# Optimization experiments

Hardware: AMD Instinct MI355X
Metric: run time of the kernel (lower is better)

The kernel has to match this reference:

```python
import jax, jax.numpy as jnp
import numpy as np

D_MODEL = 2048
BOTTLENECK = 64
EPS = 1e-5  # torch LayerNorm default


def setup_inputs() -> dict:
    key = jax.random.key(0)
    k = jax.random.split(key, 7)
    x = jax.random.normal(k[0], (4, 4096, D_MODEL), dtype=jnp.float32)
    # LayerNorm params
    ln_gamma = jnp.ones((D_MODEL,), dtype=jnp.float32)
    ln_beta = jnp.zeros((D_MODEL,), dtype=jnp.float32)
    # down_proj: Linear(d_model -> bottleneck); torch weight shape [out, in]
    w_down = jax.random.normal(k[1], (BOTTLENECK, D_MODEL), dtype=jnp.float32) * (1.0 / np.sqrt(D_MODEL))
    b_down = jax.random.normal(k[2], (BOTTLENECK,), dtype=jnp.float32) * 0.01
    # up_proj: Linear(bottleneck -> d_model)
    w_up = jax.random.normal(k[3], (D_MODEL, BOTTLENECK), dtype=jnp.float32) * (1.0 / np.sqrt(BOTTLENECK))
    b_up = jax.random.normal(k[4], (D_MODEL,), dtype=jnp.float32) * 0.01
    return {"x": x, "ln_gamma": ln_gamma, "ln_beta": ln_beta,
            "w_down": w_down, "b_down": b_down, "w_up": w_up, "b_up": b_up}


def reference(x, ln_gamma, ln_beta, w_down, b_down, w_up, b_up):
    # adapter_layernorm_option == 'in': LayerNorm first
    mu = jnp.mean(x, axis=-1, keepdims=True)
    var = jnp.mean(jnp.square(x - mu), axis=-1, keepdims=True)
    xn = (x - mu) * jax.lax.rsqrt(var + EPS) * ln_gamma + ln_beta
    # down-proj -> ReLU -> up-proj (scale/dropout are never applied in forward)
    down = jnp.maximum(jnp.einsum('bsd,kd->bsk', xn, w_down) + b_down, 0.0)
    out = jnp.einsum('bsk,dk->bsd', down, w_up) + b_up
    return out
```

## Files before the change

kernel.cpp:

```cpp
#include <hip/hip_runtime.h>


typedef __attribute__((ext_vector_type(8))) short short8;
typedef __attribute__((ext_vector_type(4))) float f32x4;

#define D_MODEL 2048
#define BNECK   64
#define EPS     1e-5f
#define NCHUNK  32

__device__ inline short f2bf(float f) {
    unsigned int u = __builtin_bit_cast(unsigned int, f);
    unsigned int r = (u + 0x7fffu + ((u >> 16) & 1u)) >> 16;
    return (short)r;
}
__device__ inline float bf2f(short s) {
    unsigned int u = ((unsigned int)(unsigned short)s) << 16;
    return __builtin_bit_cast(float, u);
}

__global__ __launch_bounds__(256) void prep_kernel(
    const float* __restrict__ w_down, const float* __restrict__ gamma,
    const float* __restrict__ beta,   const float* __restrict__ b_down,
    const float* __restrict__ w_up,
    short* __restrict__ wg_perm, short* __restrict__ wup_perm,
    float* __restrict__ s_out, float* __restrict__ c_out)
{
    __shared__ float rs[4], rc[4];
    int b = blockIdx.x;
    if (b < BNECK) {
        int n = b, nf = n >> 4;
        float ps = 0.f, pc = 0.f;
        for (int d = threadIdx.x; d < D_MODEL; d += 256) {
            float wv = w_down[n * D_MODEL + d];
            short h  = f2bf(wv * gamma[d]);
            int t = d >> 5, kg = (d >> 3) & 3, e = d & 7;
            int l = kg * 16 + (n & 15);
            wg_perm[(size_t)((nf * 64 + t) * 64 + l) * 8 + e] = h;
            ps += bf2f(h);
            pc  = fmaf(wv, beta[d], pc);
        }
        for (int o = 32; o > 0; o >>= 1) {
            ps += __shfl_down(ps, o, 64);
            pc += __shfl_down(pc, o, 64);
        }
        int wid = threadIdx.x >> 6, lane = threadIdx.x & 63;
        if (lane == 0) { rs[wid] = ps; rc[wid] = pc; }
        __syncthreads();
        if (threadIdx.x == 0) {
            s_out[n] = rs[0] + rs[1] + rs[2] + rs[3];
            c_out[n] = rc[0] + rc[1] + rc[2] + rc[3] + b_down[n];
        }
    } else {
        for (int j = (b - BNECK) * 256 + threadIdx.x; j < D_MODEL * BNECK;
             j += 64 * 256) {
            int d = j >> 6, kn = j & 63;
            int b16 = d >> 4, h2 = kn >> 5, e = kn & 7;
            int l = ((kn >> 3) & 3) * 16 + (d & 15);
            wup_perm[(size_t)((b16 * 2 + h2) * 64 + l) * 8 + e] = f2bf(w_up[j]);
        }
    }
}

__global__ __launch_bounds__(256, 4) void adapter_kernel(
    const float* __restrict__ x,    const float* __restrict__ b_up,
    const short* __restrict__ wg_perm, const short* __restrict__ wup_perm,
    const float* __restrict__ s_v,  const float* __restrict__ c_v,
    float* __restrict__ out)
{
    __shared__ __align__(16) char xbuf[2][4096];
    __shared__ __align__(16) char tilebuf[2048];
    __shared__ float stats2[16][2];

    const int wid  = threadIdx.x >> 6;
    const int lane = threadIdx.x & 63;
    const int r    = lane & 15;
    const int g    = lane >> 4;
    const int row0 = blockIdx.x * 16;
    const int swz  = (r & 7) << 4;

    const int srow = wid * 4 + g;
    const int scol = r * 16;
    const char* xsrc = (const char*)x
        + ((size_t)(row0 + srow) * D_MODEL) * 4 + scol;
    char* const swdst = &xbuf[0][0] + srow * 256 + (scol ^ ((srow & 7) << 4));

    const short* wbase = wg_perm + (size_t)(wid * 64) * 512 + lane * 8;

    f32x4  xr[4];
    short8 wb[2][2];
    f32x4  acc = (f32x4){0.f, 0.f, 0.f, 0.f};
    float  ssum = 0.f, ssq = 0.f;

    auto LDX = [&](int c) { return *(const f32x4*)(xsrc + c * 256); };
    auto LDW = [&](int c, short8* w) {
        w[0] = *(const short8*)(wbase + (size_t)(c * 2 + 0) * 512);
        w[1] = *(const short8*)(wbase + (size_t)(c * 2 + 1) * 512);
    };
    auto STATS_WRITE = [&](int c, const f32x4& v) {
        ssum += (v.x + v.y) + (v.z + v.w);
        ssq = fmaf(v.x, v.x, ssq); ssq = fmaf(v.y, v.y, ssq);
        ssq = fmaf(v.z, v.z, ssq); ssq = fmaf(v.w, v.w, ssq);
        *(f32x4*)(swdst + (size_t)(c & 1) * 4096) = v;
    };

    xr[0] = LDX(0); xr[1] = LDX(1); xr[2] = LDX(2);
    LDW(0, wb[0]);
    STATS_WRITE(0, xr[0]);

#pragma unroll
    for (int c = 0; c < NCHUNK; ++c) {
        if (c + 3 < NCHUNK) xr[(c + 3) & 3] = LDX(c + 3);
        if (c + 1 < NCHUNK) LDW(c + 1, wb[(c + 1) & 1]);
        asm volatile("s_waitcnt lgkmcnt(0)\n\ts_barrier" ::: "memory");
        if (c + 1 < NCHUNK) STATS_WRITE(c + 1, xr[(c + 1) & 3]);

        const char* bp = &xbuf[c & 1][0];
        const short8* w = wb[c & 1];
#pragma unroll
        for (int kb = 0; kb < 2; ++kb) {
            int cb = kb * 128 + g * 32;
            f32x4 xa = *(const f32x4*)(bp + r * 256 + ( cb        ^ swz));
            f32x4 xb = *(const f32x4*)(bp + r * 256 + ((cb + 16)  ^ swz));
            short8 af;
            af[0] = f2bf(xa.x); af[1] = f2bf(xa.y);
            af[2] = f2bf(xa.z); af[3] = f2bf(xa.w);
            af[4] = f2bf(xb.x); af[5] = f2bf(xb.y);
            af[6] = f2bf(xb.z); af[7] = f2bf(xb.w);
            acc = __builtin_amdgcn_mfma_f32_16x16x32_bf16(af, w[kb], acc, 0, 0, 0);
        }
    }

#pragma unroll
    for (int m = 1; m < 16; m <<= 1) {
        ssum += __shfl_xor(ssum, m, 64);
        ssq  += __shfl_xor(ssq , m, 64);
    }
    float mu   = ssum * (1.f / D_MODEL);
    float rstd = rsqrtf(ssq * (1.f / D_MODEL) - mu * mu + EPS);
    if (r == 0) { stats2[srow][0] = mu; stats2[srow][1] = rstd; }
    __syncthreads();

    {
        int   n  = wid * 16 + r;
        float sn = s_v[n], cn = c_v[n];
#pragma unroll
        for (int reg = 0; reg < 4; ++reg) {
            int   m = g * 4 + reg;
            float v = fmaf(stats2[m][1], acc[reg] - stats2[m][0] * sn, cn);
            v = fmaxf(v, 0.f);
            *(short*)(tilebuf + ((m * 128 + n * 2) ^ ((m & 7) << 4))) = f2bf(v);
        }
    }
    __syncthreads();

    short8 bd0 = *(const short8*)(tilebuf + ((r * 128 +  0 + g * 16) ^ swz));
    short8 bd1 = *(const short8*)(tilebuf + ((r * 128 + 64 + g * 16) ^ swz));

    const short* wupl = wup_perm + lane * 8;
    float* outr = out + (size_t)(row0 + r) * D_MODEL;

    short8 ua[2], ub[2];
    {
        int b16 = wid * 32;
        ua[0] = *(const short8*)(wupl + (size_t)(b16 * 2 + 0) * 512);
        ub[0] = *(const short8*)(wupl + (size_t)(b16 * 2 + 1) * 512);
    }
#pragma unroll
    for (int i = 0; i < 32; ++i) {
        int cur = i & 1;
        if (i < 31) {
            int b16 = wid * 32 + i + 1;
            ua[cur ^ 1] = *(const short8*)(wupl + (size_t)(b16 * 2 + 0) * 512);
            ub[cur ^ 1] = *(const short8*)(wupl + (size_t)(b16 * 2 + 1) * 512);
        }
        f32x4 o = (f32x4){0.f, 0.f, 0.f, 0.f};
        o = __builtin_amdgcn_mfma_f32_16x16x32_bf16(ua[cur], bd0, o, 0, 0, 0);
        o = __builtin_amdgcn_mfma_f32_16x16x32_bf16(ub[cur], bd1, o, 0, 0, 0);
        int dbase = (wid * 32 + i) * 16;
        f32x4 bu = *(const f32x4*)(b_up + dbase + g * 4);
        o += bu;
        *(f32x4*)(outr + dbase + g * 4) = o;
    }
}

extern "C" void kernel_launch(void* const* d_in, const int* in_sizes, int n_in,
                              void* d_out, int out_size, void* d_ws, size_t ws_size,
                              hipStream_t stream) {
    const float* x      = (const float*)d_in[0];
    const float* gamma  = (const float*)d_in[1];
    const float* beta   = (const float*)d_in[2];
    const float* w_down = (const float*)d_in[3];
    const float* b_down = (const float*)d_in[4];
    const float* w_up   = (const float*)d_in[5];
    const float* b_up   = (const float*)d_in[6];
    float* out = (float*)d_out;

    char* ws = (char*)d_ws;
    short* wg_perm  = (short*)ws;
    short* wup_perm = (short*)(ws + 262144);
    float* s_v  = (float*)(ws + 524288);
    float* c_v  = (float*)(ws + 524544);

    prep_kernel<<<128, 256, 0, stream>>>(w_down, gamma, beta, b_down, w_up,
                                         wg_perm, wup_perm, s_v, c_v);
    adapter_kernel<<<1024, 256, 0, stream>>>(x, b_up, wg_perm, wup_perm,
                                             s_v, c_v, out);
}
```

Baseline: 67.99 us.

## Process 32 rows per block to reuse weight fragments across two M tiles

Each block now handles 32 rows instead of 16, with two MFMA accumulators that share each loaded down-projection and up-projection weight fragment. This halves weight traffic per row and halves the grid to 512 blocks. The bf16 conversion also switches to the HIP library intrinsic, which may map to a hardware convert instruction. In exchange, each block uses twice the LDS and more registers, which could lower occupancy, and 512 blocks gives fewer waves to hide latency on a 256-CU device.

Result: slower. 71.21 us (+4.7%).

```diff
diff --git a/kernel.cpp b/kernel.cpp
--- a/kernel.cpp
+++ b/kernel.cpp
@@ -1,4 +1,5 @@
 #include <hip/hip_runtime.h>
+#include <hip/hip_bf16.h>
 
 
 typedef __attribute__((ext_vector_type(8))) short short8;
@@ -17,6 +18,16 @@
 __device__ inline float bf2f(short s) {
     unsigned int u = ((unsigned int)(unsigned short)s) << 16;
     return __builtin_bit_cast(float, u);
+}
+__device__ inline short hbf(float f) {
+    __hip_bfloat16 h = __float2bfloat16(f);
+    return __builtin_bit_cast(short, h);
+}
+__device__ inline short8 cvt8(const f32x4& a, const f32x4& b) {
+    short8 o;
+    o[0] = hbf(a.x); o[1] = hbf(a.y); o[2] = hbf(a.z); o[3] = hbf(a.w);
+    o[4] = hbf(b.x); o[5] = hbf(b.y); o[6] = hbf(b.z); o[7] = hbf(b.w);
+    return o;
 }
 
 __global__ __launch_bounds__(256) void prep_kernel(
@@ -68,49 +79,59 @@
     const float* __restrict__ s_v,  const float* __restrict__ c_v,
     float* __restrict__ out)
 {
-    __shared__ __align__(16) char xbuf[2][4096];
-    __shared__ __align__(16) char tilebuf[2048];
-    __shared__ float stats2[16][2];
+    __shared__ __align__(16) char xbuf[2][8192];
+    __shared__ __align__(16) char tilebuf[4096];
+    __shared__ float stats2[32][2];
 
     const int wid  = threadIdx.x >> 6;
     const int lane = threadIdx.x & 63;
     const int r    = lane & 15;
     const int g    = lane >> 4;
-    const int row0 = blockIdx.x * 16;
+    const int row0 = blockIdx.x * 32;
     const int swz  = (r & 7) << 4;
 
-    const int srow = wid * 4 + g;
-    const int scol = r * 16;
+    const int sr  = wid * 8 + g * 2 + (r >> 3);
+    const int scb = (r & 7) * 32;
     const char* xsrc = (const char*)x
-        + ((size_t)(row0 + srow) * D_MODEL) * 4 + scol;
-    char* const swdst = &xbuf[0][0] + srow * 256 + (scol ^ ((srow & 7) << 4));
+        + ((size_t)(row0 + sr) * D_MODEL) * 4 + scb;
+    const int swr = (sr & 7) << 4;
+    char* const swdst0 = &xbuf[0][0] + sr * 256 + ( scb       ^ swr);
+    char* const swdst1 = &xbuf[0][0] + sr * 256 + ((scb + 16) ^ swr);
 
     const short* wbase = wg_perm + (size_t)(wid * 64) * 512 + lane * 8;
 
-    f32x4  xr[4];
+    f32x4  xr[4][2];
     short8 wb[2][2];
-    f32x4  acc = (f32x4){0.f, 0.f, 0.f, 0.f};
+    f32x4  acc0 = (f32x4){0.f, 0.f, 0.f, 0.f};
+    f32x4  acc1 = (f32x4){0.f, 0.f, 0.f, 0.f};
     float  ssum = 0.f, ssq = 0.f;
 
-    auto LDX = [&](int c) { return *(const f32x4*)(xsrc + c * 256); };
+    auto LDX = [&](int c, f32x4* o) {
+        o[0] = *(const f32x4*)(xsrc + c * 256);
+        o[1] = *(const f32x4*)(xsrc + c * 256 + 16);
+    };
     auto LDW = [&](int c, short8* w) {
         w[0] = *(const short8*)(wbase + (size_t)(c * 2 + 0) * 512);
         w[1] = *(const short8*)(wbase + (size_t)(c * 2 + 1) * 512);
     };
-    auto STATS_WRITE = [&](int c, const f32x4& v) {
-        ssum += (v.x + v.y) + (v.z + v.w);
-        ssq = fmaf(v.x, v.x, ssq); ssq = fmaf(v.y, v.y, ssq);
-        ssq = fmaf(v.z, v.z, ssq); ssq = fmaf(v.w, v.w, ssq);
-        *(f32x4*)(swdst + (size_t)(c & 1) * 4096) = v;
+    auto STATS_WRITE = [&](int c, const f32x4* v) {
+#pragma unroll
+        for (int h = 0; h < 2; ++h) {
+            ssum += (v[h].x + v[h].y) + (v[h].z + v[h].w);
+            ssq = fmaf(v[h].x, v[h].x, ssq); ssq = fmaf(v[h].y, v[h].y, ssq);
+            ssq = fmaf(v[h].z, v[h].z, ssq); ssq = fmaf(v[h].w, v[h].w, ssq);
+        }
+        *(f32x4*)(swdst0 + (size_t)(c & 1) * 8192) = v[0];
+        *(f32x4*)(swdst1 + (size_t)(c & 1) * 8192) = v[1];
     };
 
-    xr[0] = LDX(0); xr[1] = LDX(1); xr[2] = LDX(2);
+    LDX(0, xr[0]); LDX(1, xr[1]); LDX(2, xr[2]);
     LDW(0, wb[0]);
     STATS_WRITE(0, xr[0]);
 
 #pragma unroll
     for (int c = 0; c < NCHUNK; ++c) {
-        if (c + 3 < NCHUNK) xr[(c + 3) & 3] = LDX(c + 3);
+        if (c + 3 < NCHUNK) LDX(c + 3, xr[(c + 3) & 3]);
         if (c + 1 < NCHUNK) LDW(c + 1, wb[(c + 1) & 1]);
         asm volatile("s_waitcnt lgkmcnt(0)\n\ts_barrier" ::: "memory");
         if (c + 1 < NCHUNK) STATS_WRITE(c + 1, xr[(c + 1) & 3]);
@@ -120,45 +141,53 @@
 #pragma unroll
         for (int kb = 0; kb < 2; ++kb) {
             int cb = kb * 128 + g * 32;
-            f32x4 xa = *(const f32x4*)(bp + r * 256 + ( cb        ^ swz));
-            f32x4 xb = *(const f32x4*)(bp + r * 256 + ((cb + 16)  ^ swz));
-            short8 af;
-            af[0] = f2bf(xa.x); af[1] = f2bf(xa.y);
-            af[2] = f2bf(xa.z); af[3] = f2bf(xa.w);
-            af[4] = f2bf(xb.x); af[5] = f2bf(xb.y);
-            af[6] = f2bf(xb.z); af[7] = f2bf(xb.w);
-            acc = __builtin_amdgcn_mfma_f32_16x16x32_bf16(af, w[kb], acc, 0, 0, 0);
-        }
-    }
-
-#pragma unroll
-    for (int m = 1; m < 16; m <<= 1) {
+            f32x4 xa0 = *(const f32x4*)(bp + r * 256        + ( cb       ^ swz));
+            f32x4 xb0 = *(const f32x4*)(bp + r * 256        + ((cb + 16) ^ swz));
+            f32x4 xa1 = *(const f32x4*)(bp + (16 + r) * 256 + ( cb       ^ swz));
+            f32x4 xb1 = *(const f32x4*)(bp + (16 + r) * 256 + ((cb + 16) ^ swz));
+            acc0 = __builtin_amdgcn_mfma_f32_16x16x32_bf16(cvt8(xa0, xb0), w[kb], acc0, 0, 0, 0);
+            acc1 = __builtin_amdgcn_mfma_f32_16x16x32_bf16(cvt8(xa1, xb1), w[kb], acc1, 0, 0, 0);
+        }
+    }
+
+#pragma unroll
+    for (int m = 1; m < 8; m <<= 1) {
         ssum += __shfl_xor(ssum, m, 64);
         ssq  += __shfl_xor(ssq , m, 64);
     }
     float mu   = ssum * (1.f / D_MODEL);
     float rstd = rsqrtf(ssq * (1.f / D_MODEL) - mu * mu + EPS);
-    if (r == 0) { stats2[srow][0] = mu; stats2[srow][1] = rstd; }
+    if ((r & 7) == 0) { stats2[sr][0] = mu; stats2[sr][1] = rstd; }
     __syncthreads();
 
     {
         int   n  = wid * 16 + r;
         float sn = s_v[n], cn = c_v[n];
 #pragma unroll
-        for (int reg = 0; reg < 4; ++reg) {
-            int   m = g * 4 + reg;
-            float v = fmaf(stats2[m][1], acc[reg] - stats2[m][0] * sn, cn);
-            v = fmaxf(v, 0.f);
-            *(short*)(tilebuf + ((m * 128 + n * 2) ^ ((m & 7) << 4))) = f2bf(v);
+        for (int mb = 0; mb < 2; ++mb) {
+            const f32x4& a = mb ? acc1 : acc0;
+#pragma unroll
+            for (int reg = 0; reg < 4; ++reg) {
+                int   m = mb * 16 + g * 4 + reg;
+                float v = fmaf(stats2[m][1], a[reg] - stats2[m][0] * sn, cn);
+                v = fmaxf(v, 0.f);
+                *(short*)(tilebuf + ((m * 128 + n * 2) ^ ((m & 7) << 4))) = hbf(v);
+            }
         }
     }
     __syncthreads();
 
-    short8 bd0 = *(const short8*)(tilebuf + ((r * 128 +  0 + g * 16) ^ swz));
-    short8 bd1 = *(const short8*)(tilebuf + ((r * 128 + 64 + g * 16) ^ swz));
+    short8 bd[2][2];
+#pragma unroll
+    for (int tb = 0; tb < 2; ++tb) {
+        int t = tb * 16 + r;
+        bd[tb][0] = *(const short8*)(tilebuf + ((t * 128 +  0 + g * 16) ^ swz));
+        bd[tb][1] = *(const short8*)(tilebuf + ((t * 128 + 64 + g * 16) ^ swz));
+    }
 
     const short* wupl = wup_perm + lane * 8;
-    float* outr = out + (size_t)(row0 + r) * D_MODEL;
+    float* outr0 = out + (size_t)(row0 + r) * D_MODEL;
+    float* outr1 = out + (size_t)(row0 + 16 + r) * D_MODEL;
 
     short8 ua[2], ub[2];
     {
@@ -174,13 +203,18 @@
             ua[cur ^ 1] = *(const short8*)(wupl + (size_t)(b16 * 2 + 0) * 512);
             ub[cur ^ 1] = *(const short8*)(wupl + (size_t)(b16 * 2 + 1) * 512);
         }
-        f32x4 o = (f32x4){0.f, 0.f, 0.f, 0.f};
-        o = __builtin_amdgcn_mfma_f32_16x16x32_bf16(ua[cur], bd0, o, 0, 0, 0);
-        o = __builtin_amdgcn_mfma_f32_16x16x32_bf16(ub[cur], bd1, o, 0, 0, 0);
         int dbase = (wid * 32 + i) * 16;
         f32x4 bu = *(const f32x4*)(b_up + dbase + g * 4);
-        o += bu;
-        *(f32x4*)(outr + dbase + g * 4) = o;
+
+        f32x4 o0 = (f32x4){0.f, 0.f, 0.f, 0.f};
+        o0 = __builtin_amdgcn_mfma_f32_16x16x32_bf16(ua[cur], bd[0][0], o0, 0, 0, 0);
+        o0 = __builtin_amdgcn_mfma_f32_16x16x32_bf16(ub[cur], bd[0][1], o0, 0, 0, 0);
+        f32x4 o1 = (f32x4){0.f, 0.f, 0.f, 0.f};
+        o1 = __builtin_amdgcn_mfma_f32_16x16x32_bf16(ua[cur], bd[1][0], o1, 0, 0, 0);
+        o1 = __builtin_amdgcn_mfma_f32_16x16x32_bf16(ub[cur], bd[1][1], o1, 0, 0, 0);
+
+        *(f32x4*)(outr0 + dbase + g * 4) = o0 + bu;
+        *(f32x4*)(outr1 + dbase + g * 4) = o1 + bu;
     }
 }
 
@@ -204,6 +238,6 @@
 
     prep_kernel<<<128, 256, 0, stream>>>(w_down, gamma, beta, b_down, w_up,
                                          wg_perm, wup_perm, s_v, c_v);
-    adapter_kernel<<<1024, 256, 0, stream>>>(x, b_up, wg_perm, wup_perm,
-                                             s_v, c_v, out);
-}
+    adapter_kernel<<<512, 256, 0, stream>>>(x, b_up, wg_perm, wup_perm,
+                                            s_v, c_v, out);
+}
```

## Stage x as bf16 in LDS in two halves instead of per-chunk pipeline

Applied to the files above, without the earlier changes.

Replaces the 32-step per-chunk pipeline, which issued a barrier on every chunk, with two large halves. In each half every thread loads 16 float4s of x, accumulates the LayerNorm statistics, converts to bf16 once and writes a swizzled 32KB LDS tile; the MFMA loop then reads bf16 fragments directly from LDS. Two accumulators interleave the MFMAs to break the dependency chain, and the conversion uses the HIP bf16 intrinsic. This removes most barriers and the repeated fp32-to-bf16 conversion on the read side. In exchange it adds more registers and LDS per block, which may lower occupancy, and there is less overlap between global loads and compute.

New measurement: 75.62 us. 11.2% more time.

```diff
diff --git a/kernel.cpp b/kernel.cpp
--- a/kernel.cpp
+++ b/kernel.cpp
@@ -1,4 +1,5 @@
 #include <hip/hip_runtime.h>
+#include <hip/hip_bf16.h>
 
 
 typedef __attribute__((ext_vector_type(8))) short short8;
@@ -7,7 +8,6 @@
 #define D_MODEL 2048
 #define BNECK   64
 #define EPS     1e-5f
-#define NCHUNK  32
 
 __device__ inline short f2bf(float f) {
     unsigned int u = __builtin_bit_cast(unsigned int, f);
@@ -17,6 +17,10 @@
 __device__ inline float bf2f(short s) {
     unsigned int u = ((unsigned int)(unsigned short)s) << 16;
     return __builtin_bit_cast(float, u);
+}
+__device__ inline short hbf(float f) {
+    __hip_bfloat16 h = __float2bfloat16(f);
+    return __builtin_bit_cast(short, h);
 }
 
 __global__ __launch_bounds__(256) void prep_kernel(
@@ -68,68 +72,70 @@
     const float* __restrict__ s_v,  const float* __restrict__ c_v,
     float* __restrict__ out)
 {
-    __shared__ __align__(16) char xbuf[2][4096];
+    __shared__ __align__(16) short xlds[16 * 1024];
     __shared__ __align__(16) char tilebuf[2048];
     __shared__ float stats2[16][2];
 
-    const int wid  = threadIdx.x >> 6;
-    const int lane = threadIdx.x & 63;
+    const int tid  = threadIdx.x;
+    const int wid  = tid >> 6;
+    const int lane = tid & 63;
     const int r    = lane & 15;
     const int g    = lane >> 4;
     const int row0 = blockIdx.x * 16;
     const int swz  = (r & 7) << 4;
-
-    const int srow = wid * 4 + g;
-    const int scol = r * 16;
-    const char* xsrc = (const char*)x
-        + ((size_t)(row0 + srow) * D_MODEL) * 4 + scol;
-    char* const swdst = &xbuf[0][0] + srow * 256 + (scol ^ ((srow & 7) << 4));
+    char* const ldsb = (char*)xlds;
+
+    const int srow = tid >> 4, sj = tid & 15;
+    const float* xsrc = x + (size_t)(row0 + srow) * D_MODEL + sj * 64;
+    const int wbyte0 = srow * 2048 + sj * 128;
+    const int wswz   = ((srow ^ (sj >> 1)) & 7) << 4;
+
+    float ssum = 0.f, ssq = 0.f;
+
+    auto STAGE_HALF = [&](int half) {
+        f32x4 v[16];
+#pragma unroll
+        for (int q = 0; q < 16; ++q)
+            v[q] = *(const f32x4*)(xsrc + half * 1024 + q * 4);
+#pragma unroll
+        for (int q = 0; q < 16; ++q) {
+            ssum += (v[q].x + v[q].y) + (v[q].z + v[q].w);
+            ssq = fmaf(v[q].x, v[q].x, ssq); ssq = fmaf(v[q].y, v[q].y, ssq);
+            ssq = fmaf(v[q].z, v[q].z, ssq); ssq = fmaf(v[q].w, v[q].w, ssq);
+        }
+#pragma unroll
+        for (int i = 0; i < 8; ++i) {
+            const f32x4 a = v[2 * i], b = v[2 * i + 1];
+            short8 u;
+            u[0] = hbf(a.x); u[1] = hbf(a.y); u[2] = hbf(a.z); u[3] = hbf(a.w);
+            u[4] = hbf(b.x); u[5] = hbf(b.y); u[6] = hbf(b.z); u[7] = hbf(b.w);
+            *(short8*)(ldsb + wbyte0 + ((i * 16) ^ wswz)) = u;
+        }
+    };
 
     const short* wbase = wg_perm + (size_t)(wid * 64) * 512 + lane * 8;
-
-    f32x4  xr[4];
-    short8 wb[2][2];
-    f32x4  acc = (f32x4){0.f, 0.f, 0.f, 0.f};
-    float  ssum = 0.f, ssq = 0.f;
-
-    auto LDX = [&](int c) { return *(const f32x4*)(xsrc + c * 256); };
-    auto LDW = [&](int c, short8* w) {
-        w[0] = *(const short8*)(wbase + (size_t)(c * 2 + 0) * 512);
-        w[1] = *(const short8*)(wbase + (size_t)(c * 2 + 1) * 512);
+    f32x4 accA = (f32x4){0.f, 0.f, 0.f, 0.f};
+    f32x4 accB = (f32x4){0.f, 0.f, 0.f, 0.f};
+
+    auto COMPUTE_HALF = [&](int half) {
+#pragma unroll 8
+        for (int s = 0; s < 32; ++s) {
+            int cb = s * 64 + g * 16;
+            int ra = r * 2048 + (cb ^ (((r ^ (s >> 2)) & 7) << 4));
+            short8 af = *(const short8*)(ldsb + ra);
+            short8 w  = *(const short8*)(wbase + (size_t)(half * 32 + s) * 512);
+            if (s & 1)
+                accB = __builtin_amdgcn_mfma_f32_16x16x32_bf16(af, w, accB, 0, 0, 0);
+            else
+                accA = __builtin_amdgcn_mfma_f32_16x16x32_bf16(af, w, accA, 0, 0, 0);
+        }
     };
-    auto STATS_WRITE = [&](int c, const f32x4& v) {
-        ssum += (v.x + v.y) + (v.z + v.w);
-        ssq = fmaf(v.x, v.x, ssq); ssq = fmaf(v.y, v.y, ssq);
-        ssq = fmaf(v.z, v.z, ssq); ssq = fmaf(v.w, v.w, ssq);
-        *(f32x4*)(swdst + (size_t)(c & 1) * 4096) = v;
-    };
-
-    xr[0] = LDX(0); xr[1] = LDX(1); xr[2] = LDX(2);
-    LDW(0, wb[0]);
-    STATS_WRITE(0, xr[0]);
-
-#pragma unroll
-    for (int c = 0; c < NCHUNK; ++c) {
-        if (c + 3 < NCHUNK) xr[(c + 3) & 3] = LDX(c + 3);
-        if (c + 1 < NCHUNK) LDW(c + 1, wb[(c + 1) & 1]);
-        asm volatile("s_waitcnt lgkmcnt(0)\n\ts_barrier" ::: "memory");
-        if (c + 1 < NCHUNK) STATS_WRITE(c + 1, xr[(c + 1) & 3]);
-
-        const char* bp = &xbuf[c & 1][0];
-        const short8* w = wb[c & 1];
-#pragma unroll
-        for (int kb = 0; kb < 2; ++kb) {
-            int cb = kb * 128 + g * 32;
-            f32x4 xa = *(const f32x4*)(bp + r * 256 + ( cb        ^ swz));
-            f32x4 xb = *(const f32x4*)(bp + r * 256 + ((cb + 16)  ^ swz));
-            short8 af;
-            af[0] = f2bf(xa.x); af[1] = f2bf(xa.y);
-            af[2] = f2bf(xa.z); af[3] = f2bf(xa.w);
-            af[4] = f2bf(xb.x); af[5] = f2bf(xb.y);
-            af[6] = f2bf(xb.z); af[7] = f2bf(xb.w);
-            acc = __builtin_amdgcn_mfma_f32_16x16x32_bf16(af, w[kb], acc, 0, 0, 0);
-        }
-    }
+
+    STAGE_HALF(0);
+    __syncthreads();
+    COMPUTE_HALF(0);
+    __syncthreads();
+    STAGE_HALF(1);
 
 #pragma unroll
     for (int m = 1; m < 16; m <<= 1) {
@@ -138,8 +144,11 @@
     }
     float mu   = ssum * (1.f / D_MODEL);
     float rstd = rsqrtf(ssq * (1.f / D_MODEL) - mu * mu + EPS);
-    if (r == 0) { stats2[srow][0] = mu; stats2[srow][1] = rstd; }
-    __syncthreads();
+    if ((tid & 15) == 0) { stats2[srow][0] = mu; stats2[srow][1] = rstd; }
+    __syncthreads();
+    COMPUTE_HALF(1);
+
+    f32x4 acc = accA + accB;
 
     {
         int   n  = wid * 16 + r;
@@ -149,7 +158,7 @@
             int   m = g * 4 + reg;
             float v = fmaf(stats2[m][1], acc[reg] - stats2[m][0] * sn, cn);
             v = fmaxf(v, 0.f);
-            *(short*)(tilebuf + ((m * 128 + n * 2) ^ ((m & 7) << 4))) = f2bf(v);
+            *(short*)(tilebuf + ((m * 128 + n * 2) ^ ((m & 7) << 4))) = hbf(v);
         }
     }
     __syncthreads();
@@ -179,8 +188,7 @@
         o = __builtin_amdgcn_mfma_f32_16x16x32_bf16(ub[cur], bd1, o, 0, 0, 0);
         int dbase = (wid * 32 + i) * 16;
         f32x4 bu = *(const f32x4*)(b_up + dbase + g * 4);
-        o += bu;
-        *(f32x4*)(outr + dbase + g * 4) = o;
+        *(f32x4*)(outr + dbase + g * 4) = o + bu;
     }
 }
 
```

## Stage up-proj outputs through LDS for coalesced row stores; use HIP bf16 convert

Applied to the files above, without the earlier changes.

The epilogue now writes each wave's MFMA output tiles into a padded shared-memory buffer. It then reads them back transposed, so each group of 16 lanes stores a contiguous 256-byte row segment instead of scattered 64-byte pieces across 16 rows. The manual float-to-bf16 rounding is also replaced with the HIP library conversion, which may lower to a hardware convert instruction. This adds LDS traffic, extra waits and about 16 KB more shared memory per block, which may reduce occupancy. The 65-float row padding also leaves some 16-byte LDS accesses unaligned.

Measured after the change: 70.10 us. 1.03x slower.

```diff
diff --git a/kernel.cpp b/kernel.cpp
--- a/kernel.cpp
+++ b/kernel.cpp
@@ -1,4 +1,5 @@
 #include <hip/hip_runtime.h>
+#include <hip/hip_bf16.h>
 
 
 typedef __attribute__((ext_vector_type(8))) short short8;
@@ -17,6 +18,10 @@
 __device__ inline float bf2f(short s) {
     unsigned int u = ((unsigned int)(unsigned short)s) << 16;
     return __builtin_bit_cast(float, u);
+}
+__device__ inline short hbf(float f) {
+    __hip_bfloat16 h = __float2bfloat16(f);
+    return __builtin_bit_cast(short, h);
 }
 
 __global__ __launch_bounds__(256) void prep_kernel(
@@ -71,6 +76,7 @@
     __shared__ __align__(16) char xbuf[2][4096];
     __shared__ __align__(16) char tilebuf[2048];
     __shared__ float stats2[16][2];
+    __shared__ __align__(16) float obuf[4][16][65];
 
     const int wid  = threadIdx.x >> 6;
     const int lane = threadIdx.x & 63;
@@ -123,10 +129,10 @@
             f32x4 xa = *(const f32x4*)(bp + r * 256 + ( cb        ^ swz));
             f32x4 xb = *(const f32x4*)(bp + r * 256 + ((cb + 16)  ^ swz));
             short8 af;
-            af[0] = f2bf(xa.x); af[1] = f2bf(xa.y);
-            af[2] = f2bf(xa.z); af[3] = f2bf(xa.w);
-            af[4] = f2bf(xb.x); af[5] = f2bf(xb.y);
-            af[6] = f2bf(xb.z); af[7] = f2bf(xb.w);
+            af[0] = hbf(xa.x); af[1] = hbf(xa.y);
+            af[2] = hbf(xa.z); af[3] = hbf(xa.w);
+            af[4] = hbf(xb.x); af[5] = hbf(xb.y);
+            af[6] = hbf(xb.z); af[7] = hbf(xb.w);
             acc = __builtin_amdgcn_mfma_f32_16x16x32_bf16(af, w[kb], acc, 0, 0, 0);
         }
     }
@@ -149,7 +155,7 @@
             int   m = g * 4 + reg;
             float v = fmaf(stats2[m][1], acc[reg] - stats2[m][0] * sn, cn);
             v = fmaxf(v, 0.f);
-            *(short*)(tilebuf + ((m * 128 + n * 2) ^ ((m & 7) << 4))) = f2bf(v);
+            *(short*)(tilebuf + ((m * 128 + n * 2) ^ ((m & 7) << 4))) = hbf(v);
         }
     }
     __syncthreads();
@@ -158,7 +164,9 @@
     short8 bd1 = *(const short8*)(tilebuf + ((r * 128 + 64 + g * 16) ^ swz));
 
     const short* wupl = wup_perm + lane * 8;
-    float* outr = out + (size_t)(row0 + r) * D_MODEL;
+    float (*ob)[65] = obuf[wid];
+    float* const outsec = out + (size_t)(row0 + g) * D_MODEL + wid * 512
+                        + r * 4;
 
     short8 ua[2], ub[2];
     {
@@ -167,20 +175,32 @@
         ub[0] = *(const short8*)(wupl + (size_t)(b16 * 2 + 1) * 512);
     }
 #pragma unroll
-    for (int i = 0; i < 32; ++i) {
-        int cur = i & 1;
-        if (i < 31) {
-            int b16 = wid * 32 + i + 1;
-            ua[cur ^ 1] = *(const short8*)(wupl + (size_t)(b16 * 2 + 0) * 512);
-            ub[cur ^ 1] = *(const short8*)(wupl + (size_t)(b16 * 2 + 1) * 512);
-        }
-        f32x4 o = (f32x4){0.f, 0.f, 0.f, 0.f};
-        o = __builtin_amdgcn_mfma_f32_16x16x32_bf16(ua[cur], bd0, o, 0, 0, 0);
-        o = __builtin_amdgcn_mfma_f32_16x16x32_bf16(ub[cur], bd1, o, 0, 0, 0);
-        int dbase = (wid * 32 + i) * 16;
-        f32x4 bu = *(const f32x4*)(b_up + dbase + g * 4);
-        o += bu;
-        *(f32x4*)(outr + dbase + g * 4) = o;
+    for (int sec = 0; sec < 8; ++sec) {
+#pragma unroll
+        for (int q = 0; q < 4; ++q) {
+            int i   = sec * 4 + q;
+            int cur = i & 1;
+            if (i < 31) {
+                int b16 = wid * 32 + i + 1;
+                ua[cur ^ 1] = *(const short8*)(wupl + (size_t)(b16 * 2 + 0) * 512);
+                ub[cur ^ 1] = *(const short8*)(wupl + (size_t)(b16 * 2 + 1) * 512);
+            }
+            f32x4 o = (f32x4){0.f, 0.f, 0.f, 0.f};
+            o = __builtin_amdgcn_mfma_f32_16x16x32_bf16(ua[cur], bd0, o, 0, 0, 0);
+            o = __builtin_amdgcn_mfma_f32_16x16x32_bf16(ub[cur], bd1, o, 0, 0, 0);
+            int dbase = (wid * 32 + i) * 16;
+            f32x4 bu = *(const f32x4*)(b_up + dbase + g * 4);
+            o += bu;
+            *(f32x4*)&ob[r][q * 16 + g * 4] = o;
+        }
+        asm volatile("s_waitcnt lgkmcnt(0)" ::: "memory");
+#pragma unroll
+        for (int q = 0; q < 4; ++q) {
+            int t = q * 4 + g;
+            f32x4 v = *(const f32x4*)&ob[t][r * 4];
+            *(f32x4*)(outsec + (size_t)(q * 4) * D_MODEL + sec * 64) = v;
+        }
+        asm volatile("s_waitcnt lgkmcnt(0)" ::: "memory");
     }
 }
 
```
